# Kernel tuning notes

Hardware: AMD Instinct MI355X
Metric: run time of the kernel (lower is better)

## Reference

```python
import jax, jax.numpy as jnp
import numpy as np

NU, NI, E, NNZ, NLAYERS, TOPK = 2560, 3584, 64, 200000, 2, 5
N = NU + NI
DQK = 4 * E  # Linear(dim, 4*dim)


def setup_inputs() -> dict:
    key = jax.random.key(0)
    ks = jax.random.split(key, 14)
    s = 1.0 / np.sqrt(E)
    return {
        "user_emb": jax.random.normal(ks[0], (NU, E), jnp.float32) * s,
        "item_emb": jax.random.normal(ks[1], (NI, E), jnp.float32) * s,
        "norm_rows": jax.random.randint(ks[2], (NNZ,), 0, N, jnp.int32),
        "norm_cols": jax.random.randint(ks[3], (NNZ,), 0, N, jnp.int32),
        "norm_vals": jax.random.uniform(ks[4], (NNZ,), jnp.float32) / 32.0,
        "adj_rows": jax.random.randint(ks[5], (NNZ,), 0, N, jnp.int32),
        "adj_cols": jax.random.randint(ks[6], (NNZ,), 0, N, jnp.int32),
        "adj_vals": jnp.ones((NNZ,), jnp.float32),
        "Wq": jax.random.normal(ks[7], (DQK, E), jnp.float32) * s,
        "bq": jnp.zeros((DQK,), jnp.float32),
        "Wk": jax.random.normal(ks[8], (DQK, E), jnp.float32) * s,
        "bk": jnp.zeros((DQK,), jnp.float32),
        "Wv": jax.random.normal(ks[9], (DQK, E), jnp.float32) * s,
        "bv": jnp.zeros((DQK,), jnp.float32),
    }


def reference(user_emb, item_emb, norm_rows, norm_cols, norm_vals,
              adj_rows, adj_cols, adj_vals, Wq, bq, Wk, bk, Wv, bv):
    # densified sparse adjacencies (duplicates accumulated, as COO spmm would)
    A_norm = jnp.zeros((N, N), jnp.float32).at[norm_rows, norm_cols].add(norm_vals)
    A = jnp.zeros((N, N), jnp.float32).at[adj_rows, adj_cols].add(adj_vals)

    ego = jnp.concatenate([user_emb, item_emb], axis=0)  # [N, E]
    layers = []
    att_out = None
    for _ in range(NLAYERS):
        layers.append(ego)
        # GNN propagation: sparse.mm(norm_adj, ego)
        ego = A_norm @ ego  # [N, E]
        # dense similarity + sparse-blended similarity
        sim = ego @ ego.T                      # [N, N]
        sim = sim + 0.5 * (A @ sim)            # [N, N]
        # top-K neighbor selection + gather
        _, idx = jax.lax.top_k(sim, TOPK)      # [N, K]
        sample = ego[idx]                      # [N, K, E]
        # SampleAttention: Linear(dim, 4*dim) Q/K/V, scaled dot-product over K neighbors
        q = ego @ Wq.T + bq                    # [N, 4E]
        kk = sample @ Wk.T + bk                # [N, K, 4E]
        vv = sample @ Wv.T + bv                # [N, K, 4E]
        scores = jnp.einsum('nd,nkd->nk', q, kk) / jnp.sqrt(jnp.float32(DQK))
        att = jax.nn.softmax(scores, axis=-1)
        att_out = jnp.einsum('nk,nkd->nd', att, vv)  # [N, 4E]
    mean_emb = jnp.mean(jnp.stack(layers, axis=1), axis=1)  # [N, E]
    return mean_emb[:NU], mean_emb[NU:], att_out
```

## Files before the change

kernel.cpp:

```cpp
#include <hip/hip_runtime.h>
#include <math.h>

#define NUSER 2560
#define NITEM 3584
#define NN    6144
#define EDIM  64
#define NNZ   200000
#define DQK   256
#define KTOP  5
#define SPLITS 8
#define TPS    6
#define CK     8
#define ELLW   96
#define TPB   256
#define QKV_BLOCKS 576
#define TOPK_BLOCKS (96 * SPLITS)
#define BSTR  72

typedef __attribute__((ext_vector_type(8))) short bf16x8;
typedef __attribute__((ext_vector_type(4))) float f32x4;

__device__ __forceinline__ unsigned short f2bf(float f) {
    unsigned int b = __float_as_uint(f);
    unsigned int r = (b + 0x7FFFu + ((b >> 16) & 1u)) >> 16;
    return (unsigned short)r;
}
__device__ __forceinline__ int pack2(float a, float b) {
    return (int)f2bf(a) | ((int)f2bf(b) << 16);
}
__device__ __forceinline__ void ell_unpack(long long v, int* col, float* w) {
    *col = (int)(v & 0xffffffffLL);
    *w   = __int_as_float((int)(v >> 32));
}

__global__ void build_kernel(const int* __restrict__ nr, const int* __restrict__ nc,
                             const float* __restrict__ nv,
                             const int* __restrict__ ar, const int* __restrict__ ac,
                             int* __restrict__ cnt_n, int* __restrict__ cnt_a,
                             long long* __restrict__ cv_n, int* __restrict__ cv_a) {
    int g = blockIdx.x * TPB + threadIdx.x;
    if (g < NNZ) {
        int r = __builtin_nontemporal_load(&nr[g]);
        int c = __builtin_nontemporal_load(&nc[g]);
        float v = __builtin_nontemporal_load(&nv[g]);
        int slot = atomicAdd(&cnt_n[r], 1);
        long long pk = (unsigned int)c | ((long long)(unsigned int)__float_as_int(v) << 32);
        __builtin_nontemporal_store(pk, &cv_n[r * ELLW + slot]);
    } else if (g < 2 * NNZ) {
        int h = g - NNZ;
        int r = __builtin_nontemporal_load(&ar[h]);
        int c = __builtin_nontemporal_load(&ac[h]);
        int slot = atomicAdd(&cnt_a[r], 1);
        __builtin_nontemporal_store(c, &cv_a[r * ELLW + slot]);
    }
}

__global__ __launch_bounds__(TPB) void spmm_ell_emb_kernel(
        const int* __restrict__ cnt, const long long* __restrict__ cv,
        const float* __restrict__ user, const float* __restrict__ item,
        float* __restrict__ dst) {
    int r = blockIdx.x * 4 + (threadIdx.x >> 6);
    int lane = threadIdx.x & 63;
    int s = r * ELLW, e = s + cnt[r];
    float a[8];
#pragma unroll
    for (int u = 0; u < 8; ++u) a[u] = 0.f;
    int j = s, n8 = s + ((e - s) & ~7);
    for (; j < n8; j += 8) {
        int col[8]; float w[8];
#pragma unroll
        for (int u = 0; u < 8; ++u) ell_unpack(__builtin_nontemporal_load(&cv[j + u]), &col[u], &w[u]);
#pragma unroll
        for (int u = 0; u < 8; ++u) {
            float x = (col[u] < NUSER) ? user[col[u] * EDIM + lane]
                                       : item[(col[u] - NUSER) * EDIM + lane];
            a[u] = fmaf(w[u], x, a[u]);
        }
    }
    for (; j < e; ++j) {
        int col; float w;
        ell_unpack(__builtin_nontemporal_load(&cv[j]), &col, &w);
        float x = (col < NUSER) ? user[col * EDIM + lane] : item[(col - NUSER) * EDIM + lane];
        a[0] = fmaf(w, x, a[0]);
    }
    dst[r * EDIM + lane] = ((a[0] + a[1]) + (a[2] + a[3])) + ((a[4] + a[5]) + (a[6] + a[7]));
}

__global__ __launch_bounds__(TPB) void spmm_ell_kernel(
        const int* __restrict__ cnt, const long long* __restrict__ cv,
        const float* __restrict__ src, float* __restrict__ dst) {
    int r = blockIdx.x * 4 + (threadIdx.x >> 6);
    int lane = threadIdx.x & 63;
    int s = r * ELLW, e = s + cnt[r];
    float a[8];
#pragma unroll
    for (int u = 0; u < 8; ++u) a[u] = 0.f;
    int j = s, n8 = s + ((e - s) & ~7);
    for (; j < n8; j += 8) {
        int col[8]; float w[8];
#pragma unroll
        for (int u = 0; u < 8; ++u) ell_unpack(__builtin_nontemporal_load(&cv[j + u]), &col[u], &w[u]);
#pragma unroll
        for (int u = 0; u < 8; ++u)
            a[u] = fmaf(w[u], src[col[u] * EDIM + lane], a[u]);
    }
    for (; j < e; ++j) {
        int col; float w;
        ell_unpack(__builtin_nontemporal_load(&cv[j]), &col, &w);
        a[0] = fmaf(w, src[col * EDIM + lane], a[0]);
    }
    dst[r * EDIM + lane] = ((a[0] + a[1]) + (a[2] + a[3])) + ((a[4] + a[5]) + (a[6] + a[7]));
}

__global__ __launch_bounds__(TPB) void qm_mean_kernel(
        const int* __restrict__ cnt, const int* __restrict__ cv,
        const float* __restrict__ ego2, const float* __restrict__ ego1,
        const float* __restrict__ user, const float* __restrict__ item,
        float* __restrict__ Qm, float* __restrict__ outmean) {
    int r = blockIdx.x * 4 + (threadIdx.x >> 6);
    int lane = threadIdx.x & 63;
    int s = r * ELLW, e = s + cnt[r];
    float a[8];
#pragma unroll
    for (int u = 0; u < 8; ++u) a[u] = 0.f;
    int j = s, n8 = s + ((e - s) & ~7);
    for (; j < n8; j += 8) {
        int col[8];
#pragma unroll
        for (int u = 0; u < 8; ++u) col[u] = __builtin_nontemporal_load(&cv[j + u]);
#pragma unroll
        for (int u = 0; u < 8; ++u)
            a[u] += ego2[col[u] * EDIM + lane];
    }
    for (; j < e; ++j) {
        int col = __builtin_nontemporal_load(&cv[j]);
        a[0] += ego2[col * EDIM + lane];
    }
    float acc = ((a[0] + a[1]) + (a[2] + a[3])) + ((a[4] + a[5]) + (a[6] + a[7]));
    int o = r * EDIM + lane;
    Qm[o] = ego2[o] + 0.5f * acc;
    float e0v = (r < NUSER) ? user[o] : item[o - NUSER * EDIM];
    outmean[o] = 0.5f * (e0v + ego1[o]);
}

__device__ __forceinline__ void ins3(float v, int ci, float tv[3], int ti[3]) {
    if (v > tv[2]) {
        bool p1 = v > tv[1], p0 = v > tv[0];
        tv[2] = p1 ? tv[1] : v;  ti[2] = p1 ? ti[1] : ci;
        if (p1) { tv[1] = p0 ? tv[0] : v; ti[1] = p0 ? ti[0] : ci; }
        if (p0) { tv[0] = v; ti[0] = ci; }
    }
}

__global__ __launch_bounds__(TPB, 3) void qkv_topk_kernel(
        const float* __restrict__ ego2,
        const float* __restrict__ Wq, const float* __restrict__ bq,
        const float* __restrict__ Wk, const float* __restrict__ bk,
        const float* __restrict__ Wv, const float* __restrict__ bv,
        float* __restrict__ Qa, float* __restrict__ Ka, float* __restrict__ Va,
        const float* __restrict__ Qm,
        int* __restrict__ pidx) {
    __shared__ __align__(16) float smem[12288];
    int t = threadIdx.x;

    if (blockIdx.x < QKV_BLOCKS) {
        int tx = t & 15, ty = t >> 4;
        int id = blockIdx.x;
        int bz = id / 192, rem = id % 192, by = rem / 96, bx = rem % 96;
        const float* W; const float* b; float* out;
        if (bz == 0)      { W = Wq; b = bq; out = Qa; }
        else if (bz == 1) { W = Wk; b = bk; out = Ka; }
        else              { W = Wv; b = bv; out = Va; }
        float* As = smem;
        float* Bs = smem + 4096;
        int r0 = bx * 64, d0 = by * 128;
        {
            int r = t & 63, eb = (t >> 6) * 16;
#pragma unroll
            for (int rep = 0; rep < 4; ++rep) {
                int e0 = eb + rep * 4;
                float4 v = *(const float4*)&ego2[(r0 + r) * EDIM + e0];
                As[(e0 + 0) * 64 + r] = v.x; As[(e0 + 1) * 64 + r] = v.y;
                As[(e0 + 2) * 64 + r] = v.z; As[(e0 + 3) * 64 + r] = v.w;
            }
        }
        {
            int d = t & 127, eb = (t >> 7) * 32;
#pragma unroll
            for (int rep = 0; rep < 8; ++rep) {
                int e0 = eb + rep * 4;
                float4 v = *(const float4*)&W[(d0 + d) * EDIM + e0];
                Bs[(e0 + 0) * 128 + d] = v.x; Bs[(e0 + 1) * 128 + d] = v.y;
                Bs[(e0 + 2) * 128 + d] = v.z; Bs[(e0 + 3) * 128 + d] = v.w;
            }
        }
        __syncthreads();
        float acc[4][8];
#pragma unroll
        for (int i = 0; i < 4; ++i)
#pragma unroll
            for (int j = 0; j < 8; ++j) acc[i][j] = 0.f;
#pragma unroll 4
        for (int e = 0; e < 64; ++e) {
            float4 a  = *(const float4*)&As[e * 64 + ty * 4];
            float4 b0 = *(const float4*)&Bs[e * 128 + tx * 4];
            float4 b1 = *(const float4*)&Bs[e * 128 + 64 + tx * 4];
            float ar[4] = {a.x, a.y, a.z, a.w};
#pragma unroll
            for (int i = 0; i < 4; ++i) {
                acc[i][0] = fmaf(ar[i], b0.x, acc[i][0]);
                acc[i][1] = fmaf(ar[i], b0.y, acc[i][1]);
                acc[i][2] = fmaf(ar[i], b0.z, acc[i][2]);
                acc[i][3] = fmaf(ar[i], b0.w, acc[i][3]);
                acc[i][4] = fmaf(ar[i], b1.x, acc[i][4]);
                acc[i][5] = fmaf(ar[i], b1.y, acc[i][5]);
                acc[i][6] = fmaf(ar[i], b1.z, acc[i][6]);
                acc[i][7] = fmaf(ar[i], b1.w, acc[i][7]);
            }
        }
        float4 bias0 = *(const float4*)&b[d0 + tx * 4];
        float4 bias1 = *(const float4*)&b[d0 + 64 + tx * 4];
#pragma unroll
        for (int i = 0; i < 4; ++i) {
            int r = r0 + ty * 4 + i;
            float4 o0 = make_float4(acc[i][0] + bias0.x, acc[i][1] + bias0.y,
                                    acc[i][2] + bias0.z, acc[i][3] + bias0.w);
            float4 o1 = make_float4(acc[i][4] + bias1.x, acc[i][5] + bias1.y,
                                    acc[i][6] + bias1.z, acc[i][7] + bias1.w);
            *(float4*)&out[r * DQK + d0 + tx * 4] = o0;
            *(float4*)&out[r * DQK + d0 + 64 + tx * 4] = o1;
        }
        return;
    }

    int id = blockIdx.x - QKV_BLOCKS;
    int rb = id % 96, sp = id / 96;
    int r0 = rb * 64;
    int w = t >> 6, lane = t & 63, lq = lane >> 4, lc = lane & 15;

    short* Ah = (short*)smem;
    short* Bh = Ah + 64 * EDIM;

    {
        int row = t >> 2, seg = t & 3;
        const float4* src = (const float4*)&Qm[(size_t)(r0 + row) * EDIM + seg * 16];
        float4 f0 = src[0], f1 = src[1], f2 = src[2], f3 = src[3];
        int4 p0, p1;
        p0.x = pack2(f0.x, f0.y); p0.y = pack2(f0.z, f0.w);
        p0.z = pack2(f1.x, f1.y); p0.w = pack2(f1.z, f1.w);
        p1.x = pack2(f2.x, f2.y); p1.y = pack2(f2.z, f2.w);
        p1.z = pack2(f3.x, f3.y); p1.w = pack2(f3.z, f3.w);
        *(int4*)&Ah[row * EDIM + seg * 16] = p0;
        *(int4*)&Ah[row * EDIM + seg * 16 + 8] = p1;
    }

    float4 pa[4], pb[4];
    {
        int c0 = (sp * TPS) * 128;
#pragma unroll
        for (int rep = 0; rep < 4; ++rep) {
            int v = t + 256 * rep;
            const float4* src = (const float4*)&ego2[(size_t)(c0 + (v >> 3)) * EDIM + (v & 7) * 8];
            pa[rep] = src[0]; pb[rep] = src[1];
        }
    }

    float t3v[4][3]; int t3i[4][3];
#pragma unroll
    for (int i = 0; i < 4; ++i)
#pragma unroll
        for (int k = 0; k < 3; ++k) { t3v[i][k] = -INFINITY; t3i[i][k] = 0x7fffffff; }

    bf16x8 af0, af1;
    for (int tile = 0; tile < TPS; ++tile) {
        int c0 = (sp * TPS + tile) * 128;
        __syncthreads();
        {
#pragma unroll
            for (int rep = 0; rep < 4; ++rep) {
                int v = t + 256 * rep;
                int4 q;
                q.x = pack2(pa[rep].x, pa[rep].y); q.y = pack2(pa[rep].z, pa[rep].w);
                q.z = pack2(pb[rep].x, pb[rep].y); q.w = pack2(pb[rep].z, pb[rep].w);
                *(int4*)&Bh[(v >> 3) * BSTR + (v & 7) * 8] = q;
            }
        }
        if (tile + 1 < TPS) {
            int c1 = c0 + 128;
#pragma unroll
            for (int rep = 0; rep < 4; ++rep) {
                int v = t + 256 * rep;
                const float4* src = (const float4*)&ego2[(size_t)(c1 + (v >> 3)) * EDIM + (v & 7) * 8];
                pa[rep] = src[0]; pb[rep] = src[1];
            }
        }
        __syncthreads();
        if (tile == 0) {
            af0 = *(const bf16x8*)&Ah[(w * 16 + lc) * EDIM + lq * 8];
            af1 = *(const bf16x8*)&Ah[(w * 16 + lc) * EDIM + 32 + lq * 8];
        }

#pragma unroll
        for (int ch = 0; ch < 8; ++ch) {
            bf16x8 b0 = *(const bf16x8*)&Bh[(ch * 16 + lc) * BSTR + lq * 8];
            bf16x8 b1 = *(const bf16x8*)&Bh[(ch * 16 + lc) * BSTR + 32 + lq * 8];
            f32x4 acc = {0.f, 0.f, 0.f, 0.f};
            acc = __builtin_amdgcn_mfma_f32_16x16x32_bf16(af0, b0, acc, 0, 0, 0);
            acc = __builtin_amdgcn_mfma_f32_16x16x32_bf16(af1, b1, acc, 0, 0, 0);
            int ci = c0 + ch * 16 + lc;
#pragma unroll
            for (int reg = 0; reg < 4; ++reg)
                ins3(acc[reg], ci, t3v[reg], t3i[reg]);
        }
    }

#pragma unroll
    for (int i = 0; i < 4; ++i) {
        int row = r0 + w * 16 + lq * 4 + i;
        int ptr = 0;
        for (int k = 0; k < CK; ++k) {
            float cvv = (ptr == 0) ? t3v[i][0] : (ptr == 1) ? t3v[i][1]
                      : (ptr == 2) ? t3v[i][2] : -INFINITY;
            int   cii = (ptr == 0) ? t3i[i][0] : (ptr == 1) ? t3i[i][1]
                      : (ptr == 2) ? t3i[i][2] : 0x7fffffff;
            float bv = cvv; int bi = cii;
#pragma unroll
            for (int off = 1; off < 16; off <<= 1) {
                float ov = __shfl_xor(bv, off, 64);
                int   oi = __shfl_xor(bi, off, 64);
                if (ov > bv || (ov == bv && oi < bi)) { bv = ov; bi = oi; }
            }
            if (bv == cvv && bi == cii) ptr++;
            if (lc == 0) pidx[(row * SPLITS + sp) * CK + k] = bi;
        }
    }
}

__global__ __launch_bounds__(TPB) void attn_kernel(
        const float* __restrict__ Qm, const float* __restrict__ ego2,
        const float* __restrict__ Qa, const float* __restrict__ Ka, const float* __restrict__ Va,
        const int* __restrict__ pidx, float* __restrict__ out) {
    __shared__ float sb[4][64];
    int wv = threadIdx.x >> 6, lane = threadIdx.x & 63;
    int r = blockIdx.x * 4 + wv;
    int ci0 = pidx[r * (SPLITS * CK) + lane];
    int part = lane & 3;

    const float4* qmp = (const float4*)(Qm + (size_t)r * EDIM + part * 16);
    float4 q0 = qmp[0], q1 = qmp[1], q2 = qmp[2], q3 = qmp[3];

#pragma unroll
    for (int p = 0; p < 4; ++p) {
        int j = p * 16 + (lane >> 2);
        int c = __shfl(ci0, j, 64);
        const float4* ep = (const float4*)(ego2 + (size_t)c * EDIM + part * 16);
        float4 e0 = ep[0], e1 = ep[1], e2 = ep[2], e3 = ep[3];
        float s = 0.f;
        s = fmaf(q0.x, e0.x, s); s = fmaf(q0.y, e0.y, s); s = fmaf(q0.z, e0.z, s); s = fmaf(q0.w, e0.w, s);
        s = fmaf(q1.x, e1.x, s); s = fmaf(q1.y, e1.y, s); s = fmaf(q1.z, e1.z, s); s = fmaf(q1.w, e1.w, s);
        s = fmaf(q2.x, e2.x, s); s = fmaf(q2.y, e2.y, s); s = fmaf(q2.z, e2.z, s); s = fmaf(q2.w, e2.w, s);
        s = fmaf(q3.x, e3.x, s); s = fmaf(q3.y, e3.y, s); s = fmaf(q3.z, e3.z, s); s = fmaf(q3.w, e3.w, s);
        s += __shfl_xor(s, 1, 64);
        s += __shfl_xor(s, 2, 64);
        if (part == 0) sb[wv][j] = s;
    }
    float sv = sb[wv][lane];

    float prevv = INFINITY; int previ = -1;
    int cI[KTOP];
#pragma unroll
    for (int k = 0; k < KTOP; ++k) {
        bool adm = (sv < prevv) || (sv == prevv && ci0 > previ);
        float bv = adm ? sv : -INFINITY;
        int   bi = adm ? ci0 : 0x7fffffff;
#pragma unroll
        for (int off = 1; off < 64; off <<= 1) {
            float ov = __shfl_xor(bv, off, 64);
            int   oi = __shfl_xor(bi, off, 64);
            if (ov > bv || (ov == bv && oi < bi)) { bv = ov; bi = oi; }
        }
        cI[k] = bi; prevv = bv; previ = bi;
    }

    float4 q = *(const float4*)&Qa[r * DQK + lane * 4];
    float sc[KTOP];
#pragma unroll
    for (int k = 0; k < KTOP; ++k) {
        float4 kk = *(const float4*)&Ka[cI[k] * DQK + lane * 4];
        float p = q.x * kk.x + q.y * kk.y + q.z * kk.z + q.w * kk.w;
#pragma unroll
        for (int off = 32; off; off >>= 1) p += __shfl_xor(p, off, 64);
        sc[k] = p * 0.0625f;
    }
    float m = sc[0];
#pragma unroll
    for (int k = 1; k < KTOP; ++k) m = fmaxf(m, sc[k]);
    float wgt[KTOP], ssum = 0.f;
#pragma unroll
    for (int k = 0; k < KTOP; ++k) { wgt[k] = expf(sc[k] - m); ssum += wgt[k]; }
    float inv = 1.f / ssum;
    float4 o = make_float4(0.f, 0.f, 0.f, 0.f);
#pragma unroll
    for (int k = 0; k < KTOP; ++k) {
        float4 vv = *(const float4*)&Va[cI[k] * DQK + lane * 4];
        float a = wgt[k] * inv;
        o.x = fmaf(a, vv.x, o.x); o.y = fmaf(a, vv.y, o.y);
        o.z = fmaf(a, vv.z, o.z); o.w = fmaf(a, vv.w, o.w);
    }
    *(float4*)&out[r * DQK + lane * 4] = o;
}

extern "C" void kernel_launch(void* const* d_in, const int* in_sizes, int n_in,
                              void* d_out, int out_size, void* d_ws, size_t ws_size,
                              hipStream_t stream) {
    const float* user  = (const float*)d_in[0];
    const float* item  = (const float*)d_in[1];
    const int*   nrows = (const int*)d_in[2];
    const int*   ncols = (const int*)d_in[3];
    const float* nvals = (const float*)d_in[4];
    const int*   arows = (const int*)d_in[5];
    const int*   acols = (const int*)d_in[6];
    const float* Wq = (const float*)d_in[8];  const float* bq = (const float*)d_in[9];
    const float* Wk = (const float*)d_in[10]; const float* bk = (const float*)d_in[11];
    const float* Wv = (const float*)d_in[12]; const float* bv = (const float*)d_in[13];
    float* out = (float*)d_out;
    float* ws  = (float*)d_ws;

    const int NE  = NN * EDIM;
    const int NQK = NN * DQK;
    float* ego1 = ws;
    float* ego2 = ws + NE;
    float* Qm   = ws + 2 * NE;
    float* Qa   = ws + 3 * NE;
    float* Ka   = Qa + NQK;
    float* Va   = Ka + NQK;
    int*   pidx = (int*)(Va + NQK);

    int* ell    = (int*)Qa;
    int* cnt_n  = ell;
    int* cnt_a  = ell + 6144;
    long long* cv_n = (long long*)(ell + 12288);
    int* cv_a   = (int*)(cv_n + NN * ELLW);

    hipMemsetAsync(cnt_n, 0, 12288 * sizeof(int), stream);
    build_kernel<<<(2 * NNZ + TPB - 1) / TPB, TPB, 0, stream>>>(nrows, ncols, nvals,
                                                                arows, acols,
                                                                cnt_n, cnt_a, cv_n, cv_a);
    spmm_ell_emb_kernel<<<NN / 4, TPB, 0, stream>>>(cnt_n, cv_n, user, item, ego1);
    spmm_ell_kernel<<<NN / 4, TPB, 0, stream>>>(cnt_n, cv_n, ego1, ego2);
    qm_mean_kernel<<<NN / 4, TPB, 0, stream>>>(cnt_a, cv_a, ego2, ego1, user, item, Qm, out);
    qkv_topk_kernel<<<QKV_BLOCKS + TOPK_BLOCKS, TPB, 0, stream>>>(
        ego2, Wq, bq, Wk, bk, Wv, bv, Qa, Ka, Va, Qm, pidx);
    attn_kernel<<<NN / 4, TPB, 0, stream>>>(Qm, ego2, Qa, Ka, Va, pidx, out + NE);
}
```

Before: 204.1 us.

## Pack top-k candidates into integer keys, precompute bf16 ego, halve QKV smem

The SpMM kernel now also writes a bf16 copy of ego2, so the top-k path loads pre-converted bf16 instead of packing fp32 on every tile. The per-lane running top-3 uses packed unsigned keys: the score bits have their low 6 mantissa bits cleared and replaced by a local tile/chunk id, so insertion becomes a branch-free umax/umin network and the cross-lane merge needs one shuffle per step instead of two. The accumulator is biased by +16 so scores sort correctly as unsigned integers. The QKV GEMM stages its tile in two halves of the K dimension to shrink LDS use, and launch bounds rise to 6 for more occupancy. The costs are truncated score precision, which can change tie-breaking among near-equal scores, and the assumption that scores stay above -16.

```diff
diff --git a/kernel.cpp b/kernel.cpp
--- a/kernel.cpp
+++ b/kernel.cpp
@@ -32,6 +32,8 @@
     *col = (int)(v & 0xffffffffLL);
     *w   = __int_as_float((int)(v >> 32));
 }
+__device__ __forceinline__ unsigned umax(unsigned a, unsigned b) { return a > b ? a : b; }
+__device__ __forceinline__ unsigned umin(unsigned a, unsigned b) { return a < b ? a : b; }
 
 __global__ void build_kernel(const int* __restrict__ nr, const int* __restrict__ nc,
                              const float* __restrict__ nv,
@@ -88,7 +90,8 @@
 
 __global__ __launch_bounds__(TPB) void spmm_ell_kernel(
         const int* __restrict__ cnt, const long long* __restrict__ cv,
-        const float* __restrict__ src, float* __restrict__ dst) {
+        const float* __restrict__ src, float* __restrict__ dst,
+        unsigned short* __restrict__ dsth) {
     int r = blockIdx.x * 4 + (threadIdx.x >> 6);
     int lane = threadIdx.x & 63;
     int s = r * ELLW, e = s + cnt[r];
@@ -109,7 +112,9 @@
         ell_unpack(__builtin_nontemporal_load(&cv[j]), &col, &w);
         a[0] = fmaf(w, src[col * EDIM + lane], a[0]);
     }
-    dst[r * EDIM + lane] = ((a[0] + a[1]) + (a[2] + a[3])) + ((a[4] + a[5]) + (a[6] + a[7]));
+    float res = ((a[0] + a[1]) + (a[2] + a[3])) + ((a[4] + a[5]) + (a[6] + a[7]));
+    dst[r * EDIM + lane]  = res;
+    dsth[r * EDIM + lane] = f2bf(res);
 }
 
 __global__ __launch_bounds__(TPB) void qm_mean_kernel(
@@ -143,24 +148,15 @@
     outmean[o] = 0.5f * (e0v + ego1[o]);
 }
 
-__device__ __forceinline__ void ins3(float v, int ci, float tv[3], int ti[3]) {
-    if (v > tv[2]) {
-        bool p1 = v > tv[1], p0 = v > tv[0];
-        tv[2] = p1 ? tv[1] : v;  ti[2] = p1 ? ti[1] : ci;
-        if (p1) { tv[1] = p0 ? tv[0] : v; ti[1] = p0 ? ti[0] : ci; }
-        if (p0) { tv[0] = v; ti[0] = ci; }
-    }
-}
-
-__global__ __launch_bounds__(TPB, 3) void qkv_topk_kernel(
-        const float* __restrict__ ego2,
+__global__ __launch_bounds__(TPB, 6) void qkv_topk_kernel(
+        const float* __restrict__ ego2, const unsigned short* __restrict__ eg2h,
         const float* __restrict__ Wq, const float* __restrict__ bq,
         const float* __restrict__ Wk, const float* __restrict__ bk,
         const float* __restrict__ Wv, const float* __restrict__ bv,
         float* __restrict__ Qa, float* __restrict__ Ka, float* __restrict__ Va,
         const float* __restrict__ Qm,
         int* __restrict__ pidx) {
-    __shared__ __align__(16) float smem[12288];
+    __shared__ __align__(16) short smem[13312];
     int t = threadIdx.x;
 
     if (blockIdx.x < QKV_BLOCKS) {
@@ -171,51 +167,55 @@
         if (bz == 0)      { W = Wq; b = bq; out = Qa; }
         else if (bz == 1) { W = Wk; b = bk; out = Ka; }
         else              { W = Wv; b = bv; out = Va; }
-        float* As = smem;
-        float* Bs = smem + 4096;
+        float* As = (float*)smem;
+        float* Bs = As + 2048;
         int r0 = bx * 64, d0 = by * 128;
-        {
-            int r = t & 63, eb = (t >> 6) * 16;
-#pragma unroll
-            for (int rep = 0; rep < 4; ++rep) {
-                int e0 = eb + rep * 4;
-                float4 v = *(const float4*)&ego2[(r0 + r) * EDIM + e0];
-                As[(e0 + 0) * 64 + r] = v.x; As[(e0 + 1) * 64 + r] = v.y;
-                As[(e0 + 2) * 64 + r] = v.z; As[(e0 + 3) * 64 + r] = v.w;
-            }
-        }
-        {
-            int d = t & 127, eb = (t >> 7) * 32;
-#pragma unroll
-            for (int rep = 0; rep < 8; ++rep) {
-                int e0 = eb + rep * 4;
-                float4 v = *(const float4*)&W[(d0 + d) * EDIM + e0];
-                Bs[(e0 + 0) * 128 + d] = v.x; Bs[(e0 + 1) * 128 + d] = v.y;
-                Bs[(e0 + 2) * 128 + d] = v.z; Bs[(e0 + 3) * 128 + d] = v.w;
-            }
-        }
-        __syncthreads();
         float acc[4][8];
 #pragma unroll
         for (int i = 0; i < 4; ++i)
 #pragma unroll
             for (int j = 0; j < 8; ++j) acc[i][j] = 0.f;
+
+        for (int h = 0; h < 2; ++h) {
+            if (h) __syncthreads();
+            {
+                int r = t & 63, eb = (t >> 6) * 8;
+#pragma unroll
+                for (int rep = 0; rep < 2; ++rep) {
+                    int e0 = eb + rep * 4;
+                    float4 v = *(const float4*)&ego2[(r0 + r) * EDIM + h * 32 + e0];
+                    As[(e0 + 0) * 64 + r] = v.x; As[(e0 + 1) * 64 + r] = v.y;
+                    As[(e0 + 2) * 64 + r] = v.z; As[(e0 + 3) * 64 + r] = v.w;
+                }
+            }
+            {
+                int d = t & 127, eb = (t >> 7) * 16;
+#pragma unroll
+                for (int rep = 0; rep < 4; ++rep) {
+                    int e0 = eb + rep * 4;
+                    float4 v = *(const float4*)&W[(d0 + d) * EDIM + h * 32 + e0];
+                    Bs[(e0 + 0) * 128 + d] = v.x; Bs[(e0 + 1) * 128 + d] = v.y;
+                    Bs[(e0 + 2) * 128 + d] = v.z; Bs[(e0 + 3) * 128 + d] = v.w;
+                }
+            }
+            __syncthreads();
 #pragma unroll 4
-        for (int e = 0; e < 64; ++e) {
-            float4 a  = *(const float4*)&As[e * 64 + ty * 4];
-            float4 b0 = *(const float4*)&Bs[e * 128 + tx * 4];
-            float4 b1 = *(const float4*)&Bs[e * 128 + 64 + tx * 4];
-            float ar[4] = {a.x, a.y, a.z, a.w};
-#pragma unroll
-            for (int i = 0; i < 4; ++i) {
-                acc[i][0] = fmaf(ar[i], b0.x, acc[i][0]);
-                acc[i][1] = fmaf(ar[i], b0.y, acc[i][1]);
-                acc[i][2] = fmaf(ar[i], b0.z, acc[i][2]);
-                acc[i][3] = fmaf(ar[i], b0.w, acc[i][3]);
-                acc[i][4] = fmaf(ar[i], b1.x, acc[i][4]);
-                acc[i][5] = fmaf(ar[i], b1.y, acc[i][5]);
-                acc[i][6] = fmaf(ar[i], b1.z, acc[i][6]);
-                acc[i][7] = fmaf(ar[i], b1.w, acc[i][7]);
+            for (int e = 0; e < 32; ++e) {
+                float4 a  = *(const float4*)&As[e * 64 + ty * 4];
+                float4 b0 = *(const float4*)&Bs[e * 128 + tx * 4];
+                float4 b1 = *(const float4*)&Bs[e * 128 + 64 + tx * 4];
+                float ar[4] = {a.x, a.y, a.z, a.w};
+#pragma unroll
+                for (int i = 0; i < 4; ++i) {
+                    acc[i][0] = fmaf(ar[i], b0.x, acc[i][0]);
+                    acc[i][1] = fmaf(ar[i], b0.y, acc[i][1]);
+                    acc[i][2] = fmaf(ar[i], b0.z, acc[i][2]);
+                    acc[i][3] = fmaf(ar[i], b0.w, acc[i][3]);
+                    acc[i][4] = fmaf(ar[i], b1.x, acc[i][4]);
+                    acc[i][5] = fmaf(ar[i], b1.y, acc[i][5]);
+                    acc[i][6] = fmaf(ar[i], b1.z, acc[i][6]);
+                    acc[i][7] = fmaf(ar[i], b1.w, acc[i][7]);
+                }
             }
         }
         float4 bias0 = *(const float4*)&b[d0 + tx * 4];
@@ -254,44 +254,37 @@
         *(int4*)&Ah[row * EDIM + seg * 16 + 8] = p1;
     }
 
-    float4 pa[4], pb[4];
+    int4 pr[4];
     {
         int c0 = (sp * TPS) * 128;
 #pragma unroll
         for (int rep = 0; rep < 4; ++rep) {
             int v = t + 256 * rep;
-            const float4* src = (const float4*)&ego2[(size_t)(c0 + (v >> 3)) * EDIM + (v & 7) * 8];
-            pa[rep] = src[0]; pb[rep] = src[1];
-        }
-    }
-
-    float t3v[4][3]; int t3i[4][3];
+            pr[rep] = *(const int4*)&eg2h[(size_t)(c0 + (v >> 3)) * EDIM + (v & 7) * 8];
+        }
+    }
+
+    unsigned t3[4][3];
 #pragma unroll
     for (int i = 0; i < 4; ++i)
 #pragma unroll
-        for (int k = 0; k < 3; ++k) { t3v[i][k] = -INFINITY; t3i[i][k] = 0x7fffffff; }
-
+        for (int k = 0; k < 3; ++k) t3[i][k] = 0u;
+
+    const unsigned KMASK = 0xFFFFFFC0u;
     bf16x8 af0, af1;
     for (int tile = 0; tile < TPS; ++tile) {
-        int c0 = (sp * TPS + tile) * 128;
         __syncthreads();
-        {
+#pragma unroll
+        for (int rep = 0; rep < 4; ++rep) {
+            int v = t + 256 * rep;
+            *(int4*)&Bh[(v >> 3) * BSTR + (v & 7) * 8] = pr[rep];
+        }
+        if (tile + 1 < TPS) {
+            int c1 = (sp * TPS + tile + 1) * 128;
 #pragma unroll
             for (int rep = 0; rep < 4; ++rep) {
                 int v = t + 256 * rep;
-                int4 q;
-                q.x = pack2(pa[rep].x, pa[rep].y); q.y = pack2(pa[rep].z, pa[rep].w);
-                q.z = pack2(pb[rep].x, pb[rep].y); q.w = pack2(pb[rep].z, pb[rep].w);
-                *(int4*)&Bh[(v >> 3) * BSTR + (v & 7) * 8] = q;
-            }
-        }
-        if (tile + 1 < TPS) {
-            int c1 = c0 + 128;
-#pragma unroll
-            for (int rep = 0; rep < 4; ++rep) {
-                int v = t + 256 * rep;
-                const float4* src = (const float4*)&ego2[(size_t)(c1 + (v >> 3)) * EDIM + (v & 7) * 8];
-                pa[rep] = src[0]; pb[rep] = src[1];
+                pr[rep] = *(const int4*)&eg2h[(size_t)(c1 + (v >> 3)) * EDIM + (v & 7) * 8];
             }
         }
         __syncthreads();
@@ -300,38 +293,45 @@
             af1 = *(const bf16x8*)&Ah[(w * 16 + lc) * EDIM + 32 + lq * 8];
         }
 
+        int tb = tile * 8;
 #pragma unroll
         for (int ch = 0; ch < 8; ++ch) {
             bf16x8 b0 = *(const bf16x8*)&Bh[(ch * 16 + lc) * BSTR + lq * 8];
             bf16x8 b1 = *(const bf16x8*)&Bh[(ch * 16 + lc) * BSTR + 32 + lq * 8];
-            f32x4 acc = {0.f, 0.f, 0.f, 0.f};
+            f32x4 acc = {16.f, 16.f, 16.f, 16.f};
             acc = __builtin_amdgcn_mfma_f32_16x16x32_bf16(af0, b0, acc, 0, 0, 0);
             acc = __builtin_amdgcn_mfma_f32_16x16x32_bf16(af1, b1, acc, 0, 0, 0);
-            int ci = c0 + ch * 16 + lc;
-#pragma unroll
-            for (int reg = 0; reg < 4; ++reg)
-                ins3(acc[reg], ci, t3v[reg], t3i[reg]);
-        }
-    }
-
+            unsigned lid = (unsigned)(tb + ch);
+#pragma unroll
+            for (int reg = 0; reg < 4; ++reg) {
+                unsigned key = (__float_as_uint(acc[reg]) & KMASK) | lid;
+                unsigned v0 = t3[reg][0], v1 = t3[reg][1], v2 = t3[reg][2];
+                t3[reg][0] = umax(v0, key);
+                t3[reg][1] = umax(v1, umin(v0, key));
+                t3[reg][2] = umax(v2, umin(v1, key));
+            }
+        }
+    }
+
+    int sb128 = sp * (TPS * 128);
+    unsigned lc2 = (unsigned)(lc << 2);
 #pragma unroll
     for (int i = 0; i < 4; ++i) {
         int row = r0 + w * 16 + lq * 4 + i;
-        int ptr = 0;
+        int base = (row * SPLITS + sp) * CK;
+        unsigned a0 = t3[i][0], a1 = t3[i][1], a2 = t3[i][2];
+#pragma unroll
         for (int k = 0; k < CK; ++k) {
-            float cvv = (ptr == 0) ? t3v[i][0] : (ptr == 1) ? t3v[i][1]
-                      : (ptr == 2) ? t3v[i][2] : -INFINITY;
-            int   cii = (ptr == 0) ? t3i[i][0] : (ptr == 1) ? t3i[i][1]
-                      : (ptr == 2) ? t3i[i][2] : 0x7fffffff;
-            float bv = cvv; int bi = cii;
-#pragma unroll
-            for (int off = 1; off < 16; off <<= 1) {
-                float ov = __shfl_xor(bv, off, 64);
-                int   oi = __shfl_xor(bi, off, 64);
-                if (ov > bv || (ov == bv && oi < bi)) { bv = ov; bi = oi; }
-            }
-            if (bv == cvv && bi == cii) ptr++;
-            if (lc == 0) pidx[(row * SPLITS + sp) * CK + k] = bi;
+            unsigned vk = (a0 & KMASK) | lc2;
+            unsigned bvv = vk;
+#pragma unroll
+            for (int off = 1; off < 16; off <<= 1)
+                bvv = umax(bvv, (unsigned)__shfl_xor((int)bvv, off, 64));
+            if (vk == bvv) {
+                unsigned lid = a0 & 63u;
+                pidx[base + k] = sb128 + (int)((lid >> 3) << 7) + (int)((lid & 7) << 4) + lc;
+                a0 = a1; a1 = a2; a2 = 0u;
+            }
         }
     }
 }
@@ -435,6 +435,7 @@
     float* Ka   = Qa + NQK;
     float* Va   = Ka + NQK;
     int*   pidx = (int*)(Va + NQK);
+    unsigned short* eg2h = (unsigned short*)(pidx + NN * SPLITS * CK);
 
     int* ell    = (int*)Qa;
     int* cnt_n  = ell;
@@ -447,9 +448,9 @@
                                                                 arows, acols,
                                                                 cnt_n, cnt_a, cv_n, cv_a);
     spmm_ell_emb_kernel<<<NN / 4, TPB, 0, stream>>>(cnt_n, cv_n, user, item, ego1);
-    spmm_ell_kernel<<<NN / 4, TPB, 0, stream>>>(cnt_n, cv_n, ego1, ego2);
+    spmm_ell_kernel<<<NN / 4, TPB, 0, stream>>>(cnt_n, cv_n, ego1, ego2, eg2h);
     qm_mean_kernel<<<NN / 4, TPB, 0, stream>>>(cnt_a, cv_a, ego2, ego1, user, item, Qm, out);
     qkv_topk_kernel<<<QKV_BLOCKS + TOPK_BLOCKS, TPB, 0, stream>>>(
-        ego2, Wq, bq, Wk, bk, Wv, bv, Qa, Ka, Va, Qm, pidx);
+        ego2, eg2h, Wq, bq, Wk, bk, Wv, bv, Qa, Ka, Va, Qm, pidx);
     attn_kernel<<<NN / 4, TPB, 0, stream>>>(Qm, ego2, Qa, Ka, Va, pidx, out + NE);
 }
```

Measured after the change: 196.4 us (median of 2 runs). 1.04x faster.
